# Optimization experiments

Measured on AMD Instinct MI355X. Metric: run time of the kernel, lower is better.

The kernel has to match this reference:

```python
import jax, jax.numpy as jnp
import numpy as np

B, D, V = 1024, 512, 100000
M = 0.4
EPS = 1e-07


def setup_inputs() -> dict:
    key = jax.random.key(0)
    k1, k2, k3 = jax.random.split(key, 3)
    inp = jax.random.normal(k1, (B, D), dtype=jnp.float32)
    # xavier_uniform for (D, V): limit = sqrt(6/(D+V))
    limit = float(np.sqrt(6.0 / (D + V)))
    weight = jax.random.uniform(k2, (D, V), dtype=jnp.float32, minval=-limit, maxval=limit)
    labels = jax.random.randint(k3, (B,), 0, V, dtype=jnp.int64)
    return {"input": inp, "weight": weight, "labels": labels}


def reference(input, weight, labels):
    # L2-normalize rows of input and columns of weight (F.normalize eps=1e-12)
    x_norm = input / jnp.maximum(jnp.linalg.norm(input, axis=1, keepdims=True), 1e-12)
    w_norm = weight / jnp.maximum(jnp.linalg.norm(weight, axis=0, keepdims=True), 1e-12)
    cosine = x_norm @ w_norm                                # [B, V]
    cosine = jnp.clip(cosine, -1.0 + EPS, 1.0 - EPS)
    arcos = jnp.arccos(cosine)
    # add margin m only at the label class (one-hot add without dense one-hot)
    rows = jnp.arange(B)
    arcos = arcos.at[rows, labels].add(M)
    logits = jnp.cos(arcos)                                 # [B, V]
    # cross-entropy, mean reduction
    logz = jax.nn.logsumexp(logits, axis=1)                 # [B]
    label_logit = logits[rows, labels]                      # [B]
    loss = jnp.mean(logz - label_logit)
    return loss
```

## Files before the change

kernel.cpp:

```cpp
#include <hip/hip_runtime.h>
#include <math.h>

#define B_    1024
#define D_    512
#define V_    100000
#define NP_   100096
#define NT_   782
#define EPS_  1e-7f
#define COSM  0.9210609940028851f
#define SINM  0.3894183423086505f

typedef __bf16 bf16x8 __attribute__((ext_vector_type(8)));
typedef float  f32x4  __attribute__((ext_vector_type(4)));

struct alignas(16) US8 { unsigned short h[8]; };

__device__ __forceinline__ unsigned short f2bf(float f) {
  union { float f; unsigned u; } a; a.f = f;
  unsigned u = a.u;
  u += 0x7FFFu + ((u >> 16) & 1u);
  return (unsigned short)(u >> 16);
}

__device__ __forceinline__ void async_copy16(void* lds, const void* g) {
  __builtin_amdgcn_global_load_lds(
      (const __attribute__((address_space(1))) void*)g,
      (__attribute__((address_space(3))) void*)lds, 16, 0, 0);
}

__global__ void x_prep(const float* __restrict__ x,
                       unsigned short* __restrict__ xb,
                       float* __restrict__ S) {
  int t = threadIdx.x;
  int lane = t & 63, wave = t >> 6;
  int row = blockIdx.x * 4 + wave;
  const float* xr = x + (size_t)row * D_;
  f32x4 a = *(const f32x4*)(xr + lane * 8);
  f32x4 b = *(const f32x4*)(xr + lane * 8 + 4);
  float ss = a[0]*a[0] + a[1]*a[1] + a[2]*a[2] + a[3]*a[3]
           + b[0]*b[0] + b[1]*b[1] + b[2]*b[2] + b[3]*b[3];
#pragma unroll
  for (int off = 32; off > 0; off >>= 1) ss += __shfl_xor(ss, off, 64);
  float inv = 1.0f / fmaxf(sqrtf(ss), 1e-12f);
  US8 pk;
#pragma unroll
  for (int j = 0; j < 4; ++j) pk.h[j]     = f2bf(a[j] * inv);
#pragma unroll
  for (int j = 0; j < 4; ++j) pk.h[4 + j] = f2bf(b[j] * inv);
  *(US8*)(xb + (size_t)row * D_ + lane * 8) = pk;
  if (lane == 0) S[row] = 0.0f;
}

#define WPC 64
#define KH  256

__global__ __launch_bounds__(256) void w_prep(const float* __restrict__ w,
                                              unsigned short* __restrict__ wbT,
                                              float* __restrict__ wssq) {
  __shared__ unsigned short T[WPC][KH];
  __shared__ float sq[16][WPC];
  int t = threadIdx.x;
  int c0 = blockIdx.x * WPC;
  int colv = (t & 15) * 4;
  int rgrp = t >> 4;
  int lane = t & 63, wave = t >> 6;
  bool vok = (c0 + colv + 3) < V_;
  float ssq[4] = {0.0f, 0.0f, 0.0f, 0.0f};

  for (int h = 0; h < 2; ++h) {
    if (vok) {
#pragma unroll
      for (int it = 0; it < 16; ++it) {
        int rl = rgrp + (it << 4);
        int row = h * KH + rl;
        f32x4 v = *(const f32x4*)(w + (size_t)row * V_ + c0 + colv);
#pragma unroll
        for (int cc = 0; cc < 4; ++cc) {
          int col = colv + cc;
          ssq[cc] += v[cc] * v[cc];
          int f8 = ((col >> 2) & 7) << 3;
          T[col][rl ^ f8] = f2bf(v[cc]);
        }
      }
    } else {
#pragma unroll
      for (int it = 0; it < 16; ++it) {
        int rl = rgrp + (it << 4);
#pragma unroll
        for (int cc = 0; cc < 4; ++cc) {
          int col = colv + cc;
          int f8 = ((col >> 2) & 7) << 3;
          T[col][rl ^ f8] = 0;
        }
      }
    }
    __syncthreads();
#pragma unroll
    for (int ci = 0; ci < 8; ++ci) {
      int col = wave * 16 + ci * 2 + (lane >> 5);
      int f = (col >> 2) & 7;
      int chunk = (lane & 31) ^ f;
      US8 pk = *(const US8*)&T[col][chunk * 8];
      *(US8*)(wbT + (size_t)(c0 + col) * D_ + h * KH + (lane & 31) * 8) = pk;
    }
    __syncthreads();
  }

#pragma unroll
  for (int cc = 0; cc < 4; ++cc) sq[rgrp][colv + cc] = ssq[cc];
  __syncthreads();
  if (t < WPC && (c0 + t) < V_) {
    float tot = 0.0f;
#pragma unroll
    for (int p = 0; p < 16; ++p) tot += sq[p][t];
    wssq[c0 + t] = tot;
  }
}

#define BM 128
#define BN 128
#define BK 64
#define NKT (D_ / BK)

__global__ __launch_bounds__(256) void gemm_fused_dma(
    const unsigned short* __restrict__ xb,
    const unsigned short* __restrict__ wbT,
    const float* __restrict__ wssq,
    const int* __restrict__ labels,
    float* __restrict__ S, float* __restrict__ Lb) {
  int bid = blockIdx.x;
  int xcd = bid & 7;
  int slot = bid >> 3;
  int tn = xcd * 98 + (slot >> 3);
  int tm = slot & 7;
  if (tn >= NT_) return;
  int m0 = tm * BM, n0 = tn * BN;

  __shared__ unsigned short Ab[2][BM * BK];
  __shared__ unsigned short Bb[2][BN * BK];
  __shared__ int labT[BM];
  int t = threadIdx.x;
  if (t < BM) labT[t] = labels[m0 + t];
  int lane = t & 63;
  int q = lane >> 4, l15 = lane & 15;
  int wave = t >> 6;
  int wm = (wave & 1) * 64, wn = (wave >> 1) * 64;
  f32x4 acc[4][4] = {};

  const unsigned short* gA[4]; unsigned short* lA[4];
  const unsigned short* gB[4]; unsigned short* lB[4];
#pragma unroll
  for (int j = 0; j < 4; ++j) {
    int p = t + 256 * j;
    int m = p >> 3;
    int kc = (p & 7) ^ (m & 7);
    gA[j] = xb  + (size_t)(m0 + m) * D_ + kc * 8;
    lA[j] = &Ab[0][p * 8];
    gB[j] = wbT + (size_t)(n0 + m) * D_ + kc * 8;
    lB[j] = &Bb[0][p * 8];
  }

#pragma unroll
  for (int j = 0; j < 4; ++j) async_copy16(lA[j], gA[j]);
#pragma unroll
  for (int j = 0; j < 4; ++j) async_copy16(lB[j], gB[j]);
  __syncthreads();

  int cur = 0;
  int h = l15 & 7;
  for (int kt = 0; kt < NKT; ++kt) {
    if (kt + 1 < NKT) {
      int off = (cur ^ 1) * (BM * BK);
      int kk = (kt + 1) * BK;
#pragma unroll
      for (int j = 0; j < 4; ++j) async_copy16(lA[j] + off, gA[j] + kk);
#pragma unroll
      for (int j = 0; j < 4; ++j) async_copy16(lB[j] + off, gB[j] + kk);
    }
    const unsigned short* Ac = Ab[cur];
    const unsigned short* Bc = Bb[cur];
#pragma unroll
    for (int s = 0; s < 2; ++s) {
      int kx = s * 4 + q;
      bf16x8 af[4], bfr[4];
#pragma unroll
      for (int ri = 0; ri < 4; ++ri) {
        int row_ = wm + ri * 16 + l15;
        af[ri] = *(const bf16x8*)&Ac[(row_ * 8 + (kx ^ h)) * 8];
      }
#pragma unroll
      for (int ci = 0; ci < 4; ++ci) {
        int row_ = wn + ci * 16 + l15;
        bfr[ci] = *(const bf16x8*)&Bc[(row_ * 8 + (kx ^ h)) * 8];
      }
#pragma unroll
      for (int ri = 0; ri < 4; ++ri)
#pragma unroll
        for (int ci = 0; ci < 4; ++ci)
          acc[ri][ci] = __builtin_amdgcn_mfma_f32_16x16x32_bf16(
              af[ri], bfr[ci], acc[ri][ci], 0, 0, 0);
    }
    __syncthreads();
    cur ^= 1;
  }

  float iw[4]; int vcol[4];
#pragma unroll
  for (int ci = 0; ci < 4; ++ci) {
    int nl = wn + ci * 16 + l15;
    vcol[ci] = n0 + nl;
    iw[ci] = (vcol[ci] < V_) ? 1.0f / fmaxf(sqrtf(wssq[vcol[ci]]), 1e-12f)
                             : 0.0f;
  }
#pragma unroll
  for (int ri = 0; ri < 4; ++ri) {
#pragma unroll
    for (int reg = 0; reg < 4; ++reg) {
      int ml = wm + ri * 16 + q * 4 + reg;
      int r = m0 + ml;
      int lab = labT[ml];
      float s = 0.0f;
#pragma unroll
      for (int ci = 0; ci < 4; ++ci) {
        float cv = acc[ri][ci][reg] * iw[ci];
        cv = fminf(fmaxf(cv, -1.0f + EPS_), 1.0f - EPS_);
        float logit = cv;
        if (vcol[ci] == lab) {
          logit = cv * COSM - sqrtf(fmaxf(1.0f - cv * cv, 0.0f)) * SINM;
          Lb[r] = logit;
        }
        s += (vcol[ci] < V_) ? __expf(logit) : 0.0f;
      }
      s += __shfl_xor(s, 1, 64);
      s += __shfl_xor(s, 2, 64);
      s += __shfl_xor(s, 4, 64);
      s += __shfl_xor(s, 8, 64);
      if (l15 == 0) atomicAdd(&S[r], s);
    }
  }
}

__global__ __launch_bounds__(256) void gemm_fused_inline(
    const unsigned short* __restrict__ xb,
    const float* __restrict__ w,
    const int* __restrict__ labels,
    float* __restrict__ S, float* __restrict__ Lb) {
  int bid = blockIdx.x;
  int xcd = bid & 7;
  int slot = bid >> 3;
  int tn = xcd * 98 + (slot >> 3);
  int tm = slot & 7;
  if (tn >= NT_) return;
  int m0 = tm * BM, n0 = tn * BN;

  __shared__ unsigned short Ab[BM * BK];
  __shared__ unsigned short Bb[BN * BK];
  __shared__ float sqred[8][BN];
  __shared__ float iwL[BN];
  __shared__ int labT[BM];
  int t = threadIdx.x;
  if (t < BM) labT[t] = labels[m0 + t];
  int lane = t & 63;
  int q = lane >> 4, l15 = lane & 15;
  int wave = t >> 6;
  int wm = (wave & 1) * 64, wn = (wave >> 1) * 64;
  f32x4 acc[4][4] = {};

  const unsigned short* gA[4];
  unsigned short* lA[4];
#pragma unroll
  for (int j = 0; j < 4; ++j) {
    int p = t + 256 * j;
    int m = p >> 3;
    int kc = (p & 7) ^ (m & 7);
    gA[j] = xb + (size_t)(m0 + m) * D_ + kc * 8;
    lA[j] = Ab + p * 8;
  }

  int cg = t & 31;
  int rp = t >> 5;
  int c0l = cg * 4;
  bool vok = (n0 + c0l + 3) < V_;
  const float* wbase = w + (size_t)rp * 8 * V_ + n0 + c0l;
  unsigned short* bdst[4];
#pragma unroll
  for (int cc = 0; cc < 4; ++cc) {
    int col = c0l + cc;
    bdst[cc] = &Bb[(col * 8 + (rp ^ (col & 7))) * 8];
  }
  float ssq[4] = {0.0f, 0.0f, 0.0f, 0.0f};

  for (int kt = 0; kt < D_; kt += BK) {
#pragma unroll
    for (int j = 0; j < 4; ++j) async_copy16(lA[j], gA[j] + kt);

    f32x4 row[8];
    if (vok) {
#pragma unroll
      for (int i = 0; i < 8; ++i)
        row[i] = *(const f32x4*)(wbase + (size_t)i * V_);
    } else {
#pragma unroll
      for (int i = 0; i < 8; ++i) row[i] = f32x4{0.0f, 0.0f, 0.0f, 0.0f};
    }
#pragma unroll
    for (int cc = 0; cc < 4; ++cc) {
      US8 pk;
#pragma unroll
      for (int i = 0; i < 8; ++i) {
        float v = row[i][cc];
        ssq[cc] += v * v;
        pk.h[i] = f2bf(v);
      }
      *(US8*)bdst[cc] = pk;
    }
    wbase += (size_t)BK * V_;

    __syncthreads();
    int h = l15 & 7;
#pragma unroll
    for (int s = 0; s < 2; ++s) {
      int kx = s * 4 + q;
      bf16x8 af[4], bfr[4];
#pragma unroll
      for (int ri = 0; ri < 4; ++ri) {
        int row_ = wm + ri * 16 + l15;
        af[ri] = *(const bf16x8*)&Ab[(row_ * 8 + (kx ^ h)) * 8];
      }
#pragma unroll
      for (int ci = 0; ci < 4; ++ci) {
        int row_ = wn + ci * 16 + l15;
        bfr[ci] = *(const bf16x8*)&Bb[(row_ * 8 + (kx ^ h)) * 8];
      }
#pragma unroll
      for (int ri = 0; ri < 4; ++ri)
#pragma unroll
        for (int ci = 0; ci < 4; ++ci)
          acc[ri][ci] = __builtin_amdgcn_mfma_f32_16x16x32_bf16(
              af[ri], bfr[ci], acc[ri][ci], 0, 0, 0);
    }
    __syncthreads();
  }

#pragma unroll
  for (int cc = 0; cc < 4; ++cc) sqred[rp][c0l + cc] = ssq[cc];
  __syncthreads();
  if (t < BN) {
    float tot = 0.0f;
#pragma unroll
    for (int p = 0; p < 8; ++p) tot += sqred[p][t];
    iwL[t] = ((n0 + t) < V_) ? 1.0f / fmaxf(sqrtf(tot), 1e-12f) : 0.0f;
  }
  __syncthreads();

  float iw[4]; int vcol[4];
#pragma unroll
  for (int ci = 0; ci < 4; ++ci) {
    int nl = wn + ci * 16 + l15;
    vcol[ci] = n0 + nl;
    iw[ci] = iwL[nl];
  }
#pragma unroll
  for (int ri = 0; ri < 4; ++ri) {
#pragma unroll
    for (int reg = 0; reg < 4; ++reg) {
      int ml = wm + ri * 16 + q * 4 + reg;
      int r = m0 + ml;
      int lab = labT[ml];
      float s = 0.0f;
#pragma unroll
      for (int ci = 0; ci < 4; ++ci) {
        float cv = acc[ri][ci][reg] * iw[ci];
        cv = fminf(fmaxf(cv, -1.0f + EPS_), 1.0f - EPS_);
        float logit = cv;
        if (vcol[ci] == lab) {
          logit = cv * COSM - sqrtf(fmaxf(1.0f - cv * cv, 0.0f)) * SINM;
          Lb[r] = logit;
        }
        s += (vcol[ci] < V_) ? __expf(logit) : 0.0f;
      }
      s += __shfl_xor(s, 1, 64);
      s += __shfl_xor(s, 2, 64);
      s += __shfl_xor(s, 4, 64);
      s += __shfl_xor(s, 8, 64);
      if (l15 == 0) atomicAdd(&S[r], s);
    }
  }
}

__global__ void finalk(const float* __restrict__ S, const float* __restrict__ Lb,
                       float* __restrict__ out) {
  __shared__ float red[256];
  int t = threadIdx.x;
  float s = 0.0f;
  for (int i = t; i < B_; i += 256) s += logf(S[i]) - Lb[i];
  red[t] = s;
  __syncthreads();
  for (int o = 128; o > 0; o >>= 1) {
    if (t < o) red[t] += red[t + o];
    __syncthreads();
  }
  if (t == 0) out[0] = red[0] * (1.0f / B_);
}

extern "C" void kernel_launch(void* const* d_in, const int* in_sizes, int n_in,
                              void* d_out, int out_size, void* d_ws, size_t ws_size,
                              hipStream_t stream) {
  const float* x = (const float*)d_in[0];
  const float* w = (const float*)d_in[1];
  const int* labels = (const int*)d_in[2];
  float* out = (float*)d_out;
  char* ws = (char*)d_ws;
  unsigned short* xb = (unsigned short*)ws;
  float* S    = (float*)(ws + 1048576ull);
  float* Lb   = (float*)(ws + 1052672ull);
  float* wssq = (float*)(ws + 1056768ull);
  unsigned short* wbT = (unsigned short*)(ws + 1457152ull);
  const size_t WS_NEED = 1457152ull + (size_t)NP_ * D_ * 2ull;

  x_prep<<<256, 256, 0, stream>>>(x, xb, S);
  if (ws_size >= WS_NEED) {
    w_prep<<<NP_ / WPC, 256, 0, stream>>>(w, wbT, wssq);
    gemm_fused_dma<<<6272, 256, 0, stream>>>(xb, wbT, wssq, labels, S, Lb);
  } else {
    gemm_fused_inline<<<6272, 256, 0, stream>>>(xb, w, labels, S, Lb);
  }
  finalk<<<1, 256, 0, stream>>>(S, Lb, out);
}
```

Before: 539.5 us.

## Enlarge GEMM tile to 256x128 with 512 threads, single-buffer LDS, rework w_prep transpose

```diff
diff --git a/kernel.cpp b/kernel.cpp
--- a/kernel.cpp
+++ b/kernel.cpp
@@ -57,57 +57,51 @@
 __global__ __launch_bounds__(256) void w_prep(const float* __restrict__ w,
                                               unsigned short* __restrict__ wbT,
                                               float* __restrict__ wssq) {
-  __shared__ unsigned short T[WPC][KH];
+  __shared__ US8  T16[WPC][32];
   __shared__ float sq[16][WPC];
   int t = threadIdx.x;
   int c0 = blockIdx.x * WPC;
-  int colv = (t & 15) * 4;
-  int rgrp = t >> 4;
+  int qv = t & 15;
+  int rg = t >> 4;
+  int colv = qv * 4;
   int lane = t & 63, wave = t >> 6;
   bool vok = (c0 + colv + 3) < V_;
   float ssq[4] = {0.0f, 0.0f, 0.0f, 0.0f};
 
   for (int h = 0; h < 2; ++h) {
-    if (vok) {
-#pragma unroll
-      for (int it = 0; it < 16; ++it) {
-        int rl = rgrp + (it << 4);
-        int row = h * KH + rl;
-        f32x4 v = *(const f32x4*)(w + (size_t)row * V_ + c0 + colv);
-#pragma unroll
-        for (int cc = 0; cc < 4; ++cc) {
-          int col = colv + cc;
-          ssq[cc] += v[cc] * v[cc];
-          int f8 = ((col >> 2) & 7) << 3;
-          T[col][rl ^ f8] = f2bf(v[cc]);
+#pragma unroll
+    for (int o = 0; o < 2; ++o) {
+      int kc = rg * 2 + o;
+      int rowb = h * KH + kc * 8;
+      US8 pk[4] = {};
+      if (vok) {
+#pragma unroll
+        for (int i = 0; i < 8; ++i) {
+          f32x4 v = *(const f32x4*)(w + (size_t)(rowb + i) * V_ + c0 + colv);
+#pragma unroll
+          for (int cc = 0; cc < 4; ++cc) {
+            ssq[cc] += v[cc] * v[cc];
+            pk[cc].h[i] = f2bf(v[cc]);
+          }
         }
       }
-    } else {
-#pragma unroll
-      for (int it = 0; it < 16; ++it) {
-        int rl = rgrp + (it << 4);
-#pragma unroll
-        for (int cc = 0; cc < 4; ++cc) {
-          int col = colv + cc;
-          int f8 = ((col >> 2) & 7) << 3;
-          T[col][rl ^ f8] = 0;
-        }
-      }
+#pragma unroll
+      for (int cc = 0; cc < 4; ++cc)
+        T16[colv + cc][kc ^ qv] = pk[cc];
     }
     __syncthreads();
 #pragma unroll
     for (int ci = 0; ci < 8; ++ci) {
       int col = wave * 16 + ci * 2 + (lane >> 5);
-      int f = (col >> 2) & 7;
-      int chunk = (lane & 31) ^ f;
-      US8 pk = *(const US8*)&T[col][chunk * 8];
-      *(US8*)(wbT + (size_t)(c0 + col) * D_ + h * KH + (lane & 31) * 8) = pk;
-    }
-    __syncthreads();
-  }
-
-#pragma unroll
-  for (int cc = 0; cc < 4; ++cc) sq[rgrp][colv + cc] = ssq[cc];
+      int kc = lane & 31;
+      US8 pk = T16[col][kc ^ (col >> 2)];
+      *(US8*)(wbT + (size_t)(c0 + col) * D_ + h * KH + kc * 8) = pk;
+    }
+    __syncthreads();
+  }
+
+#pragma unroll
+  for (int cc = 0; cc < 4; ++cc) sq[rg][colv + cc] = ssq[cc];
   __syncthreads();
   if (t < WPC && (c0 + t) < V_) {
     float tot = 0.0f;
@@ -117,12 +111,12 @@
   }
 }
 
-#define BM 128
+#define BM 256
 #define BN 128
 #define BK 64
 #define NKT (D_ / BK)
 
-__global__ __launch_bounds__(256) void gemm_fused_dma(
+__global__ __launch_bounds__(512, 4) void gemm_fused_dma(
     const unsigned short* __restrict__ xb,
     const unsigned short* __restrict__ wbT,
     const float* __restrict__ wssq,
@@ -131,54 +125,49 @@
   int bid = blockIdx.x;
   int xcd = bid & 7;
   int slot = bid >> 3;
-  int tn = xcd * 98 + (slot >> 3);
-  int tm = slot & 7;
+  int tm = slot & 3;
+  int tn = xcd * 98 + (slot >> 2);
   if (tn >= NT_) return;
   int m0 = tm * BM, n0 = tn * BN;
 
-  __shared__ unsigned short Ab[2][BM * BK];
-  __shared__ unsigned short Bb[2][BN * BK];
+  __shared__ unsigned short Ab[BM * BK];
+  __shared__ unsigned short Bb[BN * BK];
   __shared__ int labT[BM];
   int t = threadIdx.x;
   if (t < BM) labT[t] = labels[m0 + t];
   int lane = t & 63;
   int q = lane >> 4, l15 = lane & 15;
   int wave = t >> 6;
-  int wm = (wave & 1) * 64, wn = (wave >> 1) * 64;
+  int wm = (wave & 3) * 64, wn = (wave >> 2) * 64;
   f32x4 acc[4][4] = {};
 
   const unsigned short* gA[4]; unsigned short* lA[4];
-  const unsigned short* gB[4]; unsigned short* lB[4];
+  const unsigned short* gB[2]; unsigned short* lB[2];
 #pragma unroll
   for (int j = 0; j < 4; ++j) {
-    int p = t + 256 * j;
+    int p = t + 512 * j;
     int m = p >> 3;
     int kc = (p & 7) ^ (m & 7);
-    gA[j] = xb  + (size_t)(m0 + m) * D_ + kc * 8;
-    lA[j] = &Ab[0][p * 8];
+    gA[j] = xb + (size_t)(m0 + m) * D_ + kc * 8;
+    lA[j] = Ab + p * 8;
+  }
+#pragma unroll
+  for (int j = 0; j < 2; ++j) {
+    int p = t + 512 * j;
+    int m = p >> 3;
+    int kc = (p & 7) ^ (m & 7);
     gB[j] = wbT + (size_t)(n0 + m) * D_ + kc * 8;
-    lB[j] = &Bb[0][p * 8];
-  }
-
-#pragma unroll
-  for (int j = 0; j < 4; ++j) async_copy16(lA[j], gA[j]);
-#pragma unroll
-  for (int j = 0; j < 4; ++j) async_copy16(lB[j], gB[j]);
-  __syncthreads();
-
-  int cur = 0;
+    lB[j] = Bb + p * 8;
+  }
+
   int h = l15 & 7;
-  for (int kt = 0; kt < NKT; ++kt) {
-    if (kt + 1 < NKT) {
-      int off = (cur ^ 1) * (BM * BK);
-      int kk = (kt + 1) * BK;
-#pragma unroll
-      for (int j = 0; j < 4; ++j) async_copy16(lA[j] + off, gA[j] + kk);
-#pragma unroll
-      for (int j = 0; j < 4; ++j) async_copy16(lB[j] + off, gB[j] + kk);
-    }
-    const unsigned short* Ac = Ab[cur];
-    const unsigned short* Bc = Bb[cur];
+  for (int kt = 0; kt < D_; kt += BK) {
+#pragma unroll
+    for (int j = 0; j < 4; ++j) async_copy16(lA[j], gA[j] + kt);
+#pragma unroll
+    for (int j = 0; j < 2; ++j) async_copy16(lB[j], gB[j] + kt);
+    __syncthreads();
+
 #pragma unroll
     for (int s = 0; s < 2; ++s) {
       int kx = s * 4 + q;
@@ -186,12 +175,12 @@
 #pragma unroll
       for (int ri = 0; ri < 4; ++ri) {
         int row_ = wm + ri * 16 + l15;
-        af[ri] = *(const bf16x8*)&Ac[(row_ * 8 + (kx ^ h)) * 8];
+        af[ri] = *(const bf16x8*)&Ab[(row_ * 8 + (kx ^ h)) * 8];
       }
 #pragma unroll
       for (int ci = 0; ci < 4; ++ci) {
         int row_ = wn + ci * 16 + l15;
-        bfr[ci] = *(const bf16x8*)&Bc[(row_ * 8 + (kx ^ h)) * 8];
+        bfr[ci] = *(const bf16x8*)&Bb[(row_ * 8 + (kx ^ h)) * 8];
       }
 #pragma unroll
       for (int ri = 0; ri < 4; ++ri)
@@ -201,7 +190,6 @@
               af[ri], bfr[ci], acc[ri][ci], 0, 0, 0);
     }
     __syncthreads();
-    cur ^= 1;
   }
 
   float iw[4]; int vcol[4];
@@ -251,15 +239,15 @@
   int tn = xcd * 98 + (slot >> 3);
   int tm = slot & 7;
   if (tn >= NT_) return;
-  int m0 = tm * BM, n0 = tn * BN;
-
-  __shared__ unsigned short Ab[BM * BK];
-  __shared__ unsigned short Bb[BN * BK];
-  __shared__ float sqred[8][BN];
-  __shared__ float iwL[BN];
-  __shared__ int labT[BM];
+  int m0 = tm * 128, n0 = tn * 128;
+
+  __shared__ unsigned short Ab[128 * 64];
+  __shared__ unsigned short Bb[128 * 64];
+  __shared__ float sqred[8][128];
+  __shared__ float iwL[128];
+  __shared__ int labT[128];
   int t = threadIdx.x;
-  if (t < BM) labT[t] = labels[m0 + t];
+  if (t < 128) labT[t] = labels[m0 + t];
   int lane = t & 63;
   int q = lane >> 4, l15 = lane & 15;
   int wave = t >> 6;
@@ -290,7 +278,7 @@
   }
   float ssq[4] = {0.0f, 0.0f, 0.0f, 0.0f};
 
-  for (int kt = 0; kt < D_; kt += BK) {
+  for (int kt = 0; kt < D_; kt += 64) {
 #pragma unroll
     for (int j = 0; j < 4; ++j) async_copy16(lA[j], gA[j] + kt);
 
@@ -314,7 +302,7 @@
       }
       *(US8*)bdst[cc] = pk;
     }
-    wbase += (size_t)BK * V_;
+    wbase += (size_t)64 * V_;
 
     __syncthreads();
     int h = l15 & 7;
@@ -345,7 +333,7 @@
 #pragma unroll
   for (int cc = 0; cc < 4; ++cc) sqred[rp][c0l + cc] = ssq[cc];
   __syncthreads();
-  if (t < BN) {
+  if (t < 128) {
     float tot = 0.0f;
 #pragma unroll
     for (int p = 0; p < 8; ++p) tot += sqred[p][t];
@@ -421,7 +409,7 @@
   x_prep<<<256, 256, 0, stream>>>(x, xb, S);
   if (ws_size >= WS_NEED) {
     w_prep<<<NP_ / WPC, 256, 0, stream>>>(w, wbT, wssq);
-    gemm_fused_dma<<<6272, 256, 0, stream>>>(xb, wbT, wssq, labels, S, Lb);
+    gemm_fused_dma<<<3136, 512, 0, stream>>>(xb, wbT, wssq, labels, S, Lb);
   } else {
     gemm_fused_inline<<<6272, 256, 0, stream>>>(xb, w, labels, S, Lb);
   }
```

New measurement: 494.2 us. 8.4% less time.
